# Performance work log

Hardware: AMD Instinct MI355X
Metric: run time of the kernel (lower is better)

## Reference

```python
import jax, jax.numpy as jnp
import numpy as np

N, E = 50000, 800000
F_IN, H = 64, 64
DEPTH, LAYERS = 3, 2


def setup_inputs() -> dict:
    key = jax.random.key(0)
    ks = jax.random.split(key, 14)
    z = jax.random.normal(ks[0], (N, F_IN), dtype=jnp.float32)
    edge_index = jax.random.randint(ks[1], (2, E), 0, N, dtype=jnp.int64)
    s = 1.0 / np.sqrt(H)
    u = lambda k, shape: jax.random.uniform(k, shape, jnp.float32, -s, s)
    return dict(
        z=z, edge_index=edge_index,
        # GRU layer 0 (input F_IN), torch gate order r,z,n
        W_ih0=u(ks[2], (3 * H, F_IN)), W_hh0=u(ks[3], (3 * H, H)),
        b_ih0=u(ks[4], (3 * H,)), b_hh0=u(ks[5], (3 * H,)),
        # GRU layer 1 (input H)
        W_ih1=u(ks[6], (3 * H, H)), W_hh1=u(ks[7], (3 * H, H)),
        b_ih1=u(ks[8], (3 * H,)), b_hh1=u(ks[9], (3 * H,)),
        # output head: Tanh -> Linear(H, 1)
        W_out=u(ks[10], (1, H)), b_out=u(ks[11], (1,)),
    )


def _mean_aggr(h, src, dst, n_nodes):
    # scatter-mean of neighbor (src) states into dst nodes
    msg = jax.ops.segment_sum(h[src], dst, num_segments=n_nodes)  # [N, F]
    cnt = jax.ops.segment_sum(jnp.ones((src.shape[0],), h.dtype), dst,
                              num_segments=n_nodes)
    return msg / jnp.maximum(cnt, 1.0)[:, None]


def _gru_cell(x, h, W_ih, W_hh, b_ih, b_hh):
    gi = x @ W_ih.T + b_ih          # [N, 3H]
    gh = h @ W_hh.T + b_hh
    i_r, i_z, i_n = jnp.split(gi, 3, axis=-1)
    h_r, h_z, h_n = jnp.split(gh, 3, axis=-1)
    r = jax.nn.sigmoid(i_r + h_r)
    zt = jax.nn.sigmoid(i_z + h_z)
    n = jnp.tanh(i_n + r * h_n)
    return (1.0 - zt) * n + zt * h


def _run_gru_layer(xs, W_ih, W_hh, b_ih, b_hh):
    # xs: [T, N, F]; returns (outputs [T, N, H], last hidden [N, H])
    h0 = jnp.zeros((xs.shape[1], W_hh.shape[1]), xs.dtype)

    def step(h, x):
        h2 = _gru_cell(x, h, W_ih, W_hh, b_ih, b_hh)
        return h2, h2

    hT, ys = jax.lax.scan(step, h0, xs)
    return ys, hT


def reference(z, edge_index, W_ih0, W_hh0, b_ih0, b_hh0,
              W_ih1, W_hh1, b_ih1, b_hh1, W_out, b_out):
    src, dst = edge_index[0], edge_index[1]
    n_nodes = z.shape[0]
    # Build the tree-depth sequence: original z followed by DEPTH rounds of
    # mean message passing (irregular gather-aggregate-scatter per depth).
    seq = [z]
    h = z
    for _ in range(DEPTH):
        h = _mean_aggr(h, src, dst, n_nodes)
        seq.append(h)
    xs = jnp.stack(seq, axis=0)  # [DEPTH+1, N, F_IN]
    ys, _ = _run_gru_layer(xs, W_ih0, W_hh0, b_ih0, b_hh0)
    _, hT = _run_gru_layer(ys, W_ih1, W_hh1, b_ih1, b_hh1)  # top layer final state
    return jnp.tanh(hT) @ W_out.T + b_out  # [N, 1]
```

## Files before the change

### kernel.cpp

```cpp
#include <hip/hip_runtime.h>
#include <hip/hip_bf16.h>

#define N_NODES 50000
#define N_EDGES 800000

typedef __attribute__((ext_vector_type(8))) short short8;
typedef __attribute__((ext_vector_type(4))) float f32x4;

__device__ __forceinline__ unsigned short f2bf_hi(float f) {
    unsigned u = __float_as_uint(f);
    unsigned r = u + 0x7fffu + ((u >> 16) & 1u);
    return (unsigned short)(r >> 16);
}
__device__ __forceinline__ float bf2f(unsigned short h) {
    return __uint_as_float(((unsigned)h) << 16);
}
__device__ __forceinline__ float u2f(unsigned u) { return __uint_as_float(u); }

__device__ __forceinline__ unsigned pack_bf2(float a, float b) {
    float2 t{a, b};
    __hip_bfloat162 r = __float22bfloat162_rn(t);
    return *reinterpret_cast<unsigned*>(&r);
}

__device__ __forceinline__ float sigm_(float v) {
    return __builtin_amdgcn_rcpf(1.0f + __expf(-v));
}
__device__ __forceinline__ float tanh2_(float a) {
    float e = __expf(-2.0f * a);
    return fmaf(2.0f, __builtin_amdgcn_rcpf(1.0f + e), -1.0f);
}


__global__ __launch_bounds__(256) void count_kernel(const int* __restrict__ ei,
                                                    int* __restrict__ deg) {
    int e = blockIdx.x * 256 + threadIdx.x;
    if (e < N_EDGES) atomicAdd(&deg[ei[N_EDGES + e]], 1);
}

__global__ __launch_bounds__(256) void scan_part(const int* __restrict__ deg,
                                                 int* __restrict__ part) {
    __shared__ int sm[256];
    int b = blockIdx.x, t = threadIdx.x;
    int s = 0;
#pragma unroll
    for (int i = 0; i < 4; ++i) {
        int idx = b * 1024 + i * 256 + t;
        if (idx < N_NODES) s += deg[idx];
    }
    sm[t] = s;
    __syncthreads();
    for (int off = 128; off; off >>= 1) {
        if (t < off) sm[t] += sm[t + off];
        __syncthreads();
    }
    if (t == 0) part[b] = sm[0];
}

__global__ __launch_bounds__(1024) void scan_final(const int* __restrict__ deg,
                                                   const int* __restrict__ part,
                                                   int* __restrict__ rowptr,
                                                   int* __restrict__ cur) {
    __shared__ int sm[1024];
    __shared__ int basep;
    int b = blockIdx.x, t = threadIdx.x;
    if (t < 64) {
        int v = (t < b) ? part[t] : 0;
#pragma unroll
        for (int off = 1; off < 64; off <<= 1) v += __shfl_xor(v, off);
        if (t == 0) basep = v;
    }
    int idx = b * 1024 + t;
    int d = (idx < N_NODES) ? deg[idx] : 0;
    sm[t] = d;
    __syncthreads();
    for (int off = 1; off < 1024; off <<= 1) {
        int u = (t >= off) ? sm[t - off] : 0;
        __syncthreads();
        sm[t] += u;
        __syncthreads();
    }
    int excl = basep + sm[t] - d;
    if (idx < N_NODES) {
        rowptr[idx] = excl;
        cur[idx] = excl;
    } else if (idx == N_NODES) {
        rowptr[idx] = excl;
    }
}

__global__ __launch_bounds__(256) void fill_kernel(const int* __restrict__ ei,
                                                   int* __restrict__ cur,
                                                   int* __restrict__ col) {
    int e = blockIdx.x * 256 + threadIdx.x;
    if (e < N_EDGES) {
        int s = ei[e];
        int d = ei[N_EDGES + e];
        int p = atomicAdd(&cur[d], 1);
        col[p] = s;
    }
}


__global__ __launch_bounds__(256) void gather_kernel(const int* __restrict__ rowptr,
                                                     const int* __restrict__ col,
                                                     const float* __restrict__ src,
                                                     float* __restrict__ dst) {
    int node = (blockIdx.x * 256 + threadIdx.x) >> 6;
    if (node >= N_NODES) return;
    const int lane = threadIdx.x & 63;
    const int g = lane >> 4;
    const int l16 = lane & 15;
    const int beg = rowptr[node], end = rowptr[node + 1];
    const float4* s4 = reinterpret_cast<const float4*>(src);

    float4 a0 = {0.f, 0.f, 0.f, 0.f}, a1 = {0.f, 0.f, 0.f, 0.f};
    float4 a2 = {0.f, 0.f, 0.f, 0.f}, a3 = {0.f, 0.f, 0.f, 0.f};
#pragma unroll 1
    for (int e = beg + 4 * g; e < end; e += 16) {
        int c0 = col[e];
        float4 v0 = s4[c0 * 16 + l16];
        a0.x += v0.x; a0.y += v0.y; a0.z += v0.z; a0.w += v0.w;
        if (e + 1 < end) {
            int c1 = col[e + 1];
            float4 v1 = s4[c1 * 16 + l16];
            a1.x += v1.x; a1.y += v1.y; a1.z += v1.z; a1.w += v1.w;
        }
        if (e + 2 < end) {
            int c2 = col[e + 2];
            float4 v2 = s4[c2 * 16 + l16];
            a2.x += v2.x; a2.y += v2.y; a2.z += v2.z; a2.w += v2.w;
        }
        if (e + 3 < end) {
            int c3 = col[e + 3];
            float4 v3 = s4[c3 * 16 + l16];
            a3.x += v3.x; a3.y += v3.y; a3.z += v3.z; a3.w += v3.w;
        }
    }
    a0.x += a1.x; a0.y += a1.y; a0.z += a1.z; a0.w += a1.w;
    a2.x += a3.x; a2.y += a3.y; a2.z += a3.z; a2.w += a3.w;
    a0.x += a2.x; a0.y += a2.y; a0.z += a2.z; a0.w += a2.w;
#pragma unroll
    for (int m = 16; m <= 32; m <<= 1) {
        a0.x += __shfl_xor(a0.x, m);
        a0.y += __shfl_xor(a0.y, m);
        a0.z += __shfl_xor(a0.z, m);
        a0.w += __shfl_xor(a0.w, m);
    }
    if (g == 0) {
        float inv = __builtin_amdgcn_rcpf(fmaxf((float)(end - beg), 1.0f));
        float4 r = {a0.x * inv, a0.y * inv, a0.z * inv, a0.w * inv};
        reinterpret_cast<float4*>(dst)[node * 16 + l16] = r;
    }
}


__global__ __launch_bounds__(256) void wprep_kernel(
    const float* __restrict__ Wih0, const float* __restrict__ Whh0,
    const float* __restrict__ Wih1, const float* __restrict__ Whh1,
    unsigned short* __restrict__ wout) {
    int idx = blockIdx.x * 256 + threadIdx.x;
    if (idx >= 49152) return;
    int e = idx & 7;
    int lane = (idx >> 3) & 63;
    int ks = (idx >> 9) & 1;
    int r = idx >> 10;
    int ct = r % 12;
    int mat = (r / 12) & 1;
    int layer = r / 24;
    const float* W = layer ? (mat ? Whh1 : Wih1) : (mat ? Whh0 : Wih0);
    int j = ct * 16 + (lane & 15);
    int k = ks * 32 + ((lane >> 4) << 3) + e;
    float v = W[j * 64 + k];
    unsigned short hi = f2bf_hi(v);
    unsigned short lo = f2bf_hi(v - bf2f(hi));
    int base = layer * 49152 + mat * 24576 + ct * 2048 + ks * 1024;
    wout[base + lane * 8 + e] = hi;
    wout[base + 512 + lane * 8 + e] = lo;
}


__device__ __forceinline__ f32x4 mfma_bf16(short8 a, short8 b, f32x4 c) {
    return __builtin_amdgcn_mfma_f32_16x16x32_bf16(a, b, c, 0, 0, 0);
}

template <int LAYER>
__device__ __forceinline__ void mfma_phase(
    int ct, int col16, int kgrp,
    const short8 (&wf)[2][2][2][2],
    float bias_a, float bias_b,
    const unsigned short (*Ahi)[72], const unsigned short (*Alo)[72],
    unsigned short (&Hhi)[2][32][72], unsigned short (&Hlo)[2][32][72],
    float (&G)[32][196], float (&Gn2)[32][68]) {
    f32x4 acc_a[2], acc_b[2];
#pragma unroll
    for (int rt = 0; rt < 2; ++rt) {
        acc_a[rt] = {bias_a, bias_a, bias_a, bias_a};
        acc_b[rt] = {bias_b, bias_b, bias_b, bias_b};
    }
#pragma unroll
    for (int rt = 0; rt < 2; ++rt) {
#pragma unroll
        for (int ks = 0; ks < 2; ++ks) {
            const int row = rt * 16 + col16;
            const int koff = ks * 32 + kgrp;
            short8 a_in_hi = *reinterpret_cast<const short8*>(&Ahi[row][koff]);
            short8 a_in_lo = *reinterpret_cast<const short8*>(&Alo[row][koff]);
            short8 a_h_hi = *reinterpret_cast<const short8*>(&Hhi[LAYER][row][koff]);
            short8 a_h_lo = *reinterpret_cast<const short8*>(&Hlo[LAYER][row][koff]);
            short8 bi0 = wf[LAYER][0][ks][0], bi1 = wf[LAYER][0][ks][1];
            short8 bh0 = wf[LAYER][1][ks][0], bh1 = wf[LAYER][1][ks][1];
            acc_a[rt] = mfma_bf16(a_in_hi, bi0, acc_a[rt]);
            acc_a[rt] = mfma_bf16(a_in_hi, bi1, acc_a[rt]);
            acc_a[rt] = mfma_bf16(a_in_lo, bi0, acc_a[rt]);
            if (ct < 8) {
                acc_a[rt] = mfma_bf16(a_h_hi, bh0, acc_a[rt]);
                acc_a[rt] = mfma_bf16(a_h_hi, bh1, acc_a[rt]);
                acc_a[rt] = mfma_bf16(a_h_lo, bh0, acc_a[rt]);
            } else {
                acc_b[rt] = mfma_bf16(a_h_hi, bh0, acc_b[rt]);
                acc_b[rt] = mfma_bf16(a_h_hi, bh1, acc_b[rt]);
                acc_b[rt] = mfma_bf16(a_h_lo, bh0, acc_b[rt]);
            }
        }
    }
    const int q4 = (kgrp >> 3) * 4;
    const int gcol = ct * 16 + col16;
#pragma unroll
    for (int rt = 0; rt < 2; ++rt) {
#pragma unroll
        for (int v = 0; v < 4; ++v) {
            int grow = rt * 16 + q4 + v;
            G[grow][gcol] = acc_a[rt][v];
            if (ct >= 8) Gn2[grow][gcol - 128] = acc_b[rt][v];
        }
    }
}

template <int LAYER>
__device__ __forceinline__ void ew_pair(
    int p,
    unsigned short (&Hhi)[2][32][72], unsigned short (&Hlo)[2][32][72],
    float (&G)[32][196], float (&Gn2)[32][68]) {
    int m = p >> 5, j0 = (p & 31) * 2;
    float2 gr = *reinterpret_cast<const float2*>(&G[m][j0]);
    float2 gz = *reinterpret_cast<const float2*>(&G[m][64 + j0]);
    float2 gn = *reinterpret_cast<const float2*>(&G[m][128 + j0]);
    float2 gm = *reinterpret_cast<const float2*>(&Gn2[m][j0]);
    unsigned hhi = *reinterpret_cast<const unsigned*>(&Hhi[LAYER][m][j0]);
    unsigned hlo = *reinterpret_cast<const unsigned*>(&Hlo[LAYER][m][j0]);
    float hold0 = u2f(hhi << 16) + u2f(hlo << 16);
    float hold1 = u2f(hhi & 0xffff0000u) + u2f(hlo & 0xffff0000u);
    float r0 = sigm_(gr.x), r1 = sigm_(gr.y);
    float z0 = sigm_(gz.x), z1 = sigm_(gz.y);
    float n0 = tanh2_(fmaf(r0, gm.x, gn.x));
    float n1 = tanh2_(fmaf(r1, gm.y, gn.y));
    float h0 = fmaf(z0, hold0 - n0, n0);
    float h1 = fmaf(z1, hold1 - n1, n1);
    unsigned phi = pack_bf2(h0, h1);
    float l0 = h0 - u2f(phi << 16);
    float l1 = h1 - u2f(phi & 0xffff0000u);
    unsigned plo = pack_bf2(l0, l1);
    *reinterpret_cast<unsigned*>(&Hhi[LAYER][m][j0]) = phi;
    *reinterpret_cast<unsigned*>(&Hlo[LAYER][m][j0]) = plo;
}

__device__ __forceinline__ void stage_pair(const float* __restrict__ xp, int nodebase,
                                           int p,
                                           unsigned short (&Xhi)[32][72],
                                           unsigned short (&Xlo)[32][72]) {
    int m = p >> 5, k0 = (p & 31) * 2;
    int node = nodebase + m;
    if (node >= N_NODES) node = N_NODES - 1;
    float2 v = *reinterpret_cast<const float2*>(xp + (size_t)node * 64 + k0);
    unsigned phi = pack_bf2(v.x, v.y);
    float l0 = v.x - u2f(phi << 16);
    float l1 = v.y - u2f(phi & 0xffff0000u);
    *reinterpret_cast<unsigned*>(&Xhi[m][k0]) = phi;
    *reinterpret_cast<unsigned*>(&Xlo[m][k0]) = pack_bf2(l0, l1);
}

__global__ __launch_bounds__(768) void gru_kernel(
    const float* __restrict__ x0, const float* __restrict__ x1,
    const float* __restrict__ x2, const float* __restrict__ x3,
    const unsigned short* __restrict__ wprep,
    const float* __restrict__ bih0, const float* __restrict__ bhh0,
    const float* __restrict__ bih1, const float* __restrict__ bhh1,
    const float* __restrict__ Wout, const float* __restrict__ bout,
    float* __restrict__ out) {
    __shared__ __align__(16) float G[32][196];
    __shared__ __align__(16) float Gn2[32][68];
    __shared__ __align__(16) unsigned short Hhi[2][32][72];
    __shared__ __align__(16) unsigned short Hlo[2][32][72];
    __shared__ __align__(16) unsigned short Xhi[32][72];
    __shared__ __align__(16) unsigned short Xlo[32][72];

    const int tid = threadIdx.x;
    const int lane = tid & 63;
    const int ct = tid >> 6;
    const int col16 = lane & 15;
    const int kgrp = (lane >> 4) << 3;
    const int nodebase = blockIdx.x * 32;

    short8 wf[2][2][2][2];
    {
        const short8* wp = reinterpret_cast<const short8*>(wprep);
#pragma unroll
        for (int layer = 0; layer < 2; ++layer)
#pragma unroll
            for (int mat = 0; mat < 2; ++mat)
#pragma unroll
                for (int ks = 0; ks < 2; ++ks)
#pragma unroll
                    for (int term = 0; term < 2; ++term)
                        wf[layer][mat][ks][term] =
                            wp[(layer * 49152 + mat * 24576 + ct * 2048 +
                                ks * 1024 + term * 512 + lane * 8) >> 3];
    }
    const int gcol = ct * 16 + col16;
    float bias0_a, bias0_b, bias1_a, bias1_b;
    if (ct < 8) {
        bias0_a = bih0[gcol] + bhh0[gcol]; bias0_b = 0.0f;
        bias1_a = bih1[gcol] + bhh1[gcol]; bias1_b = 0.0f;
    } else {
        bias0_a = bih0[gcol]; bias0_b = bhh0[gcol];
        bias1_a = bih1[gcol]; bias1_b = bhh1[gcol];
    }

    for (int i = tid; i < 2304; i += 768) {
        reinterpret_cast<unsigned*>(&Hhi[0][0][0])[i] = 0;
        reinterpret_cast<unsigned*>(&Hlo[0][0][0])[i] = 0;
    }
    stage_pair(x0, nodebase, tid, Xhi, Xlo);
    if (tid < 256) stage_pair(x0, nodebase, tid + 768, Xhi, Xlo);
    __syncthreads();

#pragma unroll 1
    for (int t = 0; t < 4; ++t) {
        mfma_phase<0>(ct, col16, kgrp, wf, bias0_a, bias0_b,
                      Xhi, Xlo, Hhi, Hlo, G, Gn2);
        __syncthreads();
        ew_pair<0>(tid, Hhi, Hlo, G, Gn2);
        if (tid < 256) ew_pair<0>(tid + 768, Hhi, Hlo, G, Gn2);
        __syncthreads();
        mfma_phase<1>(ct, col16, kgrp, wf, bias1_a, bias1_b,
                      Hhi[0], Hlo[0], Hhi, Hlo, G, Gn2);
        __syncthreads();
        if (tid < 512) {
            ew_pair<1>(tid, Hhi, Hlo, G, Gn2);
            ew_pair<1>(tid + 512, Hhi, Hlo, G, Gn2);
        } else if (t < 3) {
            const float* xn = (t == 0) ? x1 : (t == 1) ? x2 : x3;
            int q = tid - 512;
            stage_pair(xn, nodebase, q, Xhi, Xlo);
            stage_pair(xn, nodebase, q + 256, Xhi, Xlo);
            stage_pair(xn, nodebase, q + 512, Xhi, Xlo);
            stage_pair(xn, nodebase, q + 768, Xhi, Xlo);
        }
        __syncthreads();
    }

    if (tid < 512) {
        int m = tid >> 4, l16 = tid & 15;
        float acc = 0.0f;
#pragma unroll
        for (int q = 0; q < 4; ++q) {
            int j = l16 * 4 + q;
            float h = bf2f(Hhi[1][m][j]) + bf2f(Hlo[1][m][j]);
            acc = fmaf(tanh2_(h), Wout[j], acc);
        }
        acc += __shfl_down(acc, 8, 16);
        acc += __shfl_down(acc, 4, 16);
        acc += __shfl_down(acc, 2, 16);
        acc += __shfl_down(acc, 1, 16);
        int node = nodebase + m;
        if (l16 == 0 && node < N_NODES) out[node] = acc + bout[0];
    }
}

extern "C" void kernel_launch(void* const* d_in, const int* in_sizes, int n_in,
                              void* d_out, int out_size, void* d_ws, size_t ws_size,
                              hipStream_t stream) {
    const float* z    = (const float*)d_in[0];
    const int*   ei   = (const int*)d_in[1];
    const float* Wih0 = (const float*)d_in[2];
    const float* Whh0 = (const float*)d_in[3];
    const float* bih0 = (const float*)d_in[4];
    const float* bhh0 = (const float*)d_in[5];
    const float* Wih1 = (const float*)d_in[6];
    const float* Whh1 = (const float*)d_in[7];
    const float* bih1 = (const float*)d_in[8];
    const float* bhh1 = (const float*)d_in[9];
    const float* Wout = (const float*)d_in[10];
    const float* bout = (const float*)d_in[11];
    float* out = (float*)d_out;
    float* ws  = (float*)d_ws;

    float* x1 = ws;
    float* x2 = x1 + 3200000;
    float* x3 = x2 + 3200000;
    unsigned short* wprep = (unsigned short*)(x3 + 3200000);
    int* rowptr = (int*)(ws + 9600000 + 49152);
    int* deg    = rowptr + 50004;
    int* cur    = deg + 50000;
    int* col    = cur + 50000;
    int* part   = col + 800000;

    hipMemsetAsync(deg, 0, 50000 * sizeof(int), stream);

    wprep_kernel<<<192, 256, 0, stream>>>(Wih0, Whh0, Wih1, Whh1, wprep);
    count_kernel<<<(N_EDGES + 255) / 256, 256, 0, stream>>>(ei, deg);
    scan_part<<<49, 256, 0, stream>>>(deg, part);
    scan_final<<<49, 1024, 0, stream>>>(deg, part, rowptr, cur);
    fill_kernel<<<(N_EDGES + 255) / 256, 256, 0, stream>>>(ei, cur, col);

    gather_kernel<<<(N_NODES * 64 + 255) / 256, 256, 0, stream>>>(rowptr, col, z, x1);
    gather_kernel<<<(N_NODES * 64 + 255) / 256, 256, 0, stream>>>(rowptr, col, x1, x2);
    gather_kernel<<<(N_NODES * 64 + 255) / 256, 256, 0, stream>>>(rowptr, col, x2, x3);

    gru_kernel<<<(N_NODES + 31) / 32, 768, 0, stream>>>(
        z, x1, x2, x3, wprep, bih0, bhh0, bih1, bhh1, Wout, bout, out);
}
```

Before: 389.9 us.

## Store aggregated features as bf16 hi/lo pairs and gather bf16 in later hops

The gather kernels now write mean-aggregated features as split bf16 hi/lo arrays instead of fp32. Depth 2 and 3 gather only the bf16 hi part of the previous hop, which halves gather bytes per edge. The GRU kernel loads the pre-split bf16 directly instead of converting fp32 during staging. LDS row padding also changes from 72 to 76 with 8-byte reads to reduce bank conflicts. Dropping the lo part in later hops loses some precision in the aggregated features.

```diff
diff --git a/kernel.cpp b/kernel.cpp
--- a/kernel.cpp
+++ b/kernel.cpp
@@ -102,10 +102,10 @@
 }
 
 
-__global__ __launch_bounds__(256) void gather_kernel(const int* __restrict__ rowptr,
-                                                     const int* __restrict__ col,
-                                                     const float* __restrict__ src,
-                                                     float* __restrict__ dst) {
+__global__ __launch_bounds__(256) void gather_f32_kernel(
+    const int* __restrict__ rowptr, const int* __restrict__ col,
+    const float* __restrict__ src,
+    unsigned short* __restrict__ dsthi, unsigned short* __restrict__ dstlo) {
     int node = (blockIdx.x * 256 + threadIdx.x) >> 6;
     if (node >= N_NODES) return;
     const int lane = threadIdx.x & 63;
@@ -118,22 +118,18 @@
     float4 a2 = {0.f, 0.f, 0.f, 0.f}, a3 = {0.f, 0.f, 0.f, 0.f};
 #pragma unroll 1
     for (int e = beg + 4 * g; e < end; e += 16) {
-        int c0 = col[e];
-        float4 v0 = s4[c0 * 16 + l16];
+        float4 v0 = s4[col[e] * 16 + l16];
         a0.x += v0.x; a0.y += v0.y; a0.z += v0.z; a0.w += v0.w;
         if (e + 1 < end) {
-            int c1 = col[e + 1];
-            float4 v1 = s4[c1 * 16 + l16];
+            float4 v1 = s4[col[e + 1] * 16 + l16];
             a1.x += v1.x; a1.y += v1.y; a1.z += v1.z; a1.w += v1.w;
         }
         if (e + 2 < end) {
-            int c2 = col[e + 2];
-            float4 v2 = s4[c2 * 16 + l16];
+            float4 v2 = s4[col[e + 2] * 16 + l16];
             a2.x += v2.x; a2.y += v2.y; a2.z += v2.z; a2.w += v2.w;
         }
         if (e + 3 < end) {
-            int c3 = col[e + 3];
-            float4 v3 = s4[c3 * 16 + l16];
+            float4 v3 = s4[col[e + 3] * 16 + l16];
             a3.x += v3.x; a3.y += v3.y; a3.z += v3.z; a3.w += v3.w;
         }
     }
@@ -149,8 +145,61 @@
     }
     if (g == 0) {
         float inv = __builtin_amdgcn_rcpf(fmaxf((float)(end - beg), 1.0f));
-        float4 r = {a0.x * inv, a0.y * inv, a0.z * inv, a0.w * inv};
-        reinterpret_cast<float4*>(dst)[node * 16 + l16] = r;
+        float m0 = a0.x * inv, m1 = a0.y * inv, m2 = a0.z * inv, m3 = a0.w * inv;
+        unsigned h01 = pack_bf2(m0, m1), h23 = pack_bf2(m2, m3);
+        float l0 = m0 - u2f(h01 << 16), l1 = m1 - u2f(h01 & 0xffff0000u);
+        float l2 = m2 - u2f(h23 << 16), l3 = m3 - u2f(h23 & 0xffff0000u);
+        uint2 hw = {h01, h23};
+        uint2 lw = {pack_bf2(l0, l1), pack_bf2(l2, l3)};
+        reinterpret_cast<uint2*>(dsthi)[node * 16 + l16] = hw;
+        reinterpret_cast<uint2*>(dstlo)[node * 16 + l16] = lw;
+    }
+}
+
+
+__global__ __launch_bounds__(256) void gather_bf16_kernel(
+    const int* __restrict__ rowptr, const int* __restrict__ col,
+    const unsigned short* __restrict__ srchi,
+    unsigned short* __restrict__ dsthi, unsigned short* __restrict__ dstlo) {
+    int node = (blockIdx.x * 256 + threadIdx.x) >> 6;
+    if (node >= N_NODES) return;
+    const int lane = threadIdx.x & 63;
+    const int g = lane >> 4;
+    const int l16 = lane & 15;
+    const int beg = rowptr[node], end = rowptr[node + 1];
+    const uint2* s2 = reinterpret_cast<const uint2*>(srchi);
+
+    float b0 = 0.f, b1 = 0.f, b2 = 0.f, b3 = 0.f;
+    float c0 = 0.f, c1 = 0.f, c2 = 0.f, c3 = 0.f;
+#pragma unroll 1
+    for (int e = beg + 2 * g; e < end; e += 8) {
+        uint2 v = s2[col[e] * 16 + l16];
+        b0 += u2f(v.x << 16); b1 += u2f(v.x & 0xffff0000u);
+        b2 += u2f(v.y << 16); b3 += u2f(v.y & 0xffff0000u);
+        if (e + 1 < end) {
+            uint2 w = s2[col[e + 1] * 16 + l16];
+            c0 += u2f(w.x << 16); c1 += u2f(w.x & 0xffff0000u);
+            c2 += u2f(w.y << 16); c3 += u2f(w.y & 0xffff0000u);
+        }
+    }
+    b0 += c0; b1 += c1; b2 += c2; b3 += c3;
+#pragma unroll
+    for (int m = 16; m <= 32; m <<= 1) {
+        b0 += __shfl_xor(b0, m);
+        b1 += __shfl_xor(b1, m);
+        b2 += __shfl_xor(b2, m);
+        b3 += __shfl_xor(b3, m);
+    }
+    if (g == 0) {
+        float inv = __builtin_amdgcn_rcpf(fmaxf((float)(end - beg), 1.0f));
+        float m0 = b0 * inv, m1 = b1 * inv, m2 = b2 * inv, m3 = b3 * inv;
+        unsigned h01 = pack_bf2(m0, m1), h23 = pack_bf2(m2, m3);
+        float l0 = m0 - u2f(h01 << 16), l1 = m1 - u2f(h01 & 0xffff0000u);
+        float l2 = m2 - u2f(h23 << 16), l3 = m3 - u2f(h23 & 0xffff0000u);
+        uint2 hw = {h01, h23};
+        uint2 lw = {pack_bf2(l0, l1), pack_bf2(l2, l3)};
+        reinterpret_cast<uint2*>(dsthi)[node * 16 + l16] = hw;
+        reinterpret_cast<uint2*>(dstlo)[node * 16 + l16] = lw;
     }
 }
 
@@ -184,13 +233,22 @@
     return __builtin_amdgcn_mfma_f32_16x16x32_bf16(a, b, c, 0, 0, 0);
 }
 
+__device__ __forceinline__ short8 lds_read8(const unsigned short* p) {
+    union { uint2 u[2]; short8 s; } t;
+    t.u[0] = *reinterpret_cast<const uint2*>(p);
+    t.u[1] = *reinterpret_cast<const uint2*>(p + 4);
+    return t.s;
+}
+
+#define HPAD 76
+
 template <int LAYER>
 __device__ __forceinline__ void mfma_phase(
     int ct, int col16, int kgrp,
     const short8 (&wf)[2][2][2][2],
     float bias_a, float bias_b,
-    const unsigned short (*Ahi)[72], const unsigned short (*Alo)[72],
-    unsigned short (&Hhi)[2][32][72], unsigned short (&Hlo)[2][32][72],
+    const unsigned short (*Ahi)[HPAD], const unsigned short (*Alo)[HPAD],
+    unsigned short (&Hhi)[2][32][HPAD], unsigned short (&Hlo)[2][32][HPAD],
     float (&G)[32][196], float (&Gn2)[32][68]) {
     f32x4 acc_a[2], acc_b[2];
 #pragma unroll
@@ -204,10 +262,10 @@
         for (int ks = 0; ks < 2; ++ks) {
             const int row = rt * 16 + col16;
             const int koff = ks * 32 + kgrp;
-            short8 a_in_hi = *reinterpret_cast<const short8*>(&Ahi[row][koff]);
-            short8 a_in_lo = *reinterpret_cast<const short8*>(&Alo[row][koff]);
-            short8 a_h_hi = *reinterpret_cast<const short8*>(&Hhi[LAYER][row][koff]);
-            short8 a_h_lo = *reinterpret_cast<const short8*>(&Hlo[LAYER][row][koff]);
+            short8 a_in_hi = lds_read8(&Ahi[row][koff]);
+            short8 a_in_lo = lds_read8(&Alo[row][koff]);
+            short8 a_h_hi = lds_read8(&Hhi[LAYER][row][koff]);
+            short8 a_h_lo = lds_read8(&Hlo[LAYER][row][koff]);
             short8 bi0 = wf[LAYER][0][ks][0], bi1 = wf[LAYER][0][ks][1];
             short8 bh0 = wf[LAYER][1][ks][0], bh1 = wf[LAYER][1][ks][1];
             acc_a[rt] = mfma_bf16(a_in_hi, bi0, acc_a[rt]);
@@ -240,7 +298,7 @@
 template <int LAYER>
 __device__ __forceinline__ void ew_pair(
     int p,
-    unsigned short (&Hhi)[2][32][72], unsigned short (&Hlo)[2][32][72],
+    unsigned short (&Hhi)[2][32][HPAD], unsigned short (&Hlo)[2][32][HPAD],
     float (&G)[32][196], float (&Gn2)[32][68]) {
     int m = p >> 5, j0 = (p & 31) * 2;
     float2 gr = *reinterpret_cast<const float2*>(&G[m][j0]);
@@ -265,10 +323,10 @@
     *reinterpret_cast<unsigned*>(&Hlo[LAYER][m][j0]) = plo;
 }
 
-__device__ __forceinline__ void stage_pair(const float* __restrict__ xp, int nodebase,
-                                           int p,
-                                           unsigned short (&Xhi)[32][72],
-                                           unsigned short (&Xlo)[32][72]) {
+__device__ __forceinline__ void stage_pair_f32(const float* __restrict__ xp, int nodebase,
+                                               int p,
+                                               unsigned short (&Xhi)[32][HPAD],
+                                               unsigned short (&Xlo)[32][HPAD]) {
     int m = p >> 5, k0 = (p & 31) * 2;
     int node = nodebase + m;
     if (node >= N_NODES) node = N_NODES - 1;
@@ -281,8 +339,10 @@
 }
 
 __global__ __launch_bounds__(768) void gru_kernel(
-    const float* __restrict__ x0, const float* __restrict__ x1,
-    const float* __restrict__ x2, const float* __restrict__ x3,
+    const float* __restrict__ z,
+    const unsigned* __restrict__ xh1, const unsigned* __restrict__ xl1,
+    const unsigned* __restrict__ xh2, const unsigned* __restrict__ xl2,
+    const unsigned* __restrict__ xh3, const unsigned* __restrict__ xl3,
     const unsigned short* __restrict__ wprep,
     const float* __restrict__ bih0, const float* __restrict__ bhh0,
     const float* __restrict__ bih1, const float* __restrict__ bhh1,
@@ -290,10 +350,10 @@
     float* __restrict__ out) {
     __shared__ __align__(16) float G[32][196];
     __shared__ __align__(16) float Gn2[32][68];
-    __shared__ __align__(16) unsigned short Hhi[2][32][72];
-    __shared__ __align__(16) unsigned short Hlo[2][32][72];
-    __shared__ __align__(16) unsigned short Xhi[32][72];
-    __shared__ __align__(16) unsigned short Xlo[32][72];
+    __shared__ __align__(16) unsigned short Hhi[2][32][HPAD];
+    __shared__ __align__(16) unsigned short Hlo[2][32][HPAD];
+    __shared__ __align__(16) unsigned short Xhi[32][HPAD];
+    __shared__ __align__(16) unsigned short Xlo[32][HPAD];
 
     const int tid = threadIdx.x;
     const int lane = tid & 63;
@@ -327,12 +387,16 @@
         bias1_a = bih1[gcol]; bias1_b = bhh1[gcol];
     }
 
-    for (int i = tid; i < 2304; i += 768) {
-        reinterpret_cast<unsigned*>(&Hhi[0][0][0])[i] = 0;
-        reinterpret_cast<unsigned*>(&Hlo[0][0][0])[i] = 0;
-    }
-    stage_pair(x0, nodebase, tid, Xhi, Xlo);
-    if (tid < 256) stage_pair(x0, nodebase, tid + 768, Xhi, Xlo);
+    {
+        unsigned* h32 = reinterpret_cast<unsigned*>(&Hhi[0][0][0]);
+        unsigned* l32 = reinterpret_cast<unsigned*>(&Hlo[0][0][0]);
+        for (int i = tid; i < 2432; i += 768) {
+            h32[i] = 0;
+            l32[i] = 0;
+        }
+    }
+    stage_pair_f32(z, nodebase, tid, Xhi, Xlo);
+    if (tid < 256) stage_pair_f32(z, nodebase, tid + 768, Xhi, Xlo);
     __syncthreads();
 
 #pragma unroll 1
@@ -350,12 +414,18 @@
             ew_pair<1>(tid, Hhi, Hlo, G, Gn2);
             ew_pair<1>(tid + 512, Hhi, Hlo, G, Gn2);
         } else if (t < 3) {
-            const float* xn = (t == 0) ? x1 : (t == 1) ? x2 : x3;
+            const unsigned* hp = (t == 0) ? xh1 : (t == 1) ? xh2 : xh3;
+            const unsigned* lp = (t == 0) ? xl1 : (t == 1) ? xl2 : xl3;
             int q = tid - 512;
-            stage_pair(xn, nodebase, q, Xhi, Xlo);
-            stage_pair(xn, nodebase, q + 256, Xhi, Xlo);
-            stage_pair(xn, nodebase, q + 512, Xhi, Xlo);
-            stage_pair(xn, nodebase, q + 768, Xhi, Xlo);
+#pragma unroll
+            for (int i = 0; i < 4; ++i) {
+                int d = q + 256 * i;
+                int m = d >> 5, c = d & 31;
+                int node = nodebase + m;
+                if (node >= N_NODES) node = N_NODES - 1;
+                *reinterpret_cast<unsigned*>(&Xhi[m][2 * c]) = hp[node * 32 + c];
+                *reinterpret_cast<unsigned*>(&Xlo[m][2 * c]) = lp[node * 32 + c];
+            }
         }
         __syncthreads();
     }
@@ -394,13 +464,16 @@
     const float* Wout = (const float*)d_in[10];
     const float* bout = (const float*)d_in[11];
     float* out = (float*)d_out;
-    float* ws  = (float*)d_ws;
-
-    float* x1 = ws;
-    float* x2 = x1 + 3200000;
-    float* x3 = x2 + 3200000;
-    unsigned short* wprep = (unsigned short*)(x3 + 3200000);
-    int* rowptr = (int*)(ws + 9600000 + 49152);
+    unsigned* ws = (unsigned*)d_ws;
+
+    unsigned* xh1 = ws;
+    unsigned* xl1 = xh1 + 1600000;
+    unsigned* xh2 = xl1 + 1600000;
+    unsigned* xl2 = xh2 + 1600000;
+    unsigned* xh3 = xl2 + 1600000;
+    unsigned* xl3 = xh3 + 1600000;
+    unsigned short* wprep = (unsigned short*)(xl3 + 1600000);
+    int* rowptr = (int*)(wprep + 98304);
     int* deg    = rowptr + 50004;
     int* cur    = deg + 50000;
     int* col    = cur + 50000;
@@ -414,10 +487,16 @@
     scan_final<<<49, 1024, 0, stream>>>(deg, part, rowptr, cur);
     fill_kernel<<<(N_EDGES + 255) / 256, 256, 0, stream>>>(ei, cur, col);
 
-    gather_kernel<<<(N_NODES * 64 + 255) / 256, 256, 0, stream>>>(rowptr, col, z, x1);
-    gather_kernel<<<(N_NODES * 64 + 255) / 256, 256, 0, stream>>>(rowptr, col, x1, x2);
-    gather_kernel<<<(N_NODES * 64 + 255) / 256, 256, 0, stream>>>(rowptr, col, x2, x3);
+    gather_f32_kernel<<<(N_NODES * 64 + 255) / 256, 256, 0, stream>>>(
+        rowptr, col, z, (unsigned short*)xh1, (unsigned short*)xl1);
+    gather_bf16_kernel<<<(N_NODES * 64 + 255) / 256, 256, 0, stream>>>(
+        rowptr, col, (const unsigned short*)xh1,
+        (unsigned short*)xh2, (unsigned short*)xl2);
+    gather_bf16_kernel<<<(N_NODES * 64 + 255) / 256, 256, 0, stream>>>(
+        rowptr, col, (const unsigned short*)xh2,
+        (unsigned short*)xh3, (unsigned short*)xl3);
 
     gru_kernel<<<(N_NODES + 31) / 32, 768, 0, stream>>>(
-        z, x1, x2, x3, wprep, bih0, bhh0, bih1, bhh1, Wout, bout, out);
-}
+        z, xh1, xl1, xh2, xl2, xh3, xl3, wprep,
+        bih0, bhh0, bih1, bhh1, Wout, bout, out);
+}
```

Result: faster. 374.0 us (-4.1%).
